# Optimization experiments

Hardware: AMD Instinct MI355X
Metric: run time of the kernel (lower is better)

The kernel has to match this reference:

```python
import jax, jax.numpy as jnp
import numpy as np

N, E = 50000, 1600000
IN_DIM, EMBED, OUT = 512, 128, 64


def setup_inputs() -> dict:
    key = jax.random.key(0)
    k = jax.random.split(key, 8)
    x = jax.random.normal(k[0], (N, IN_DIM), dtype=jnp.float32)
    edge_index = jax.random.randint(k[1], (2, E), 0, N, dtype=jnp.int32)
    W_dense = jax.random.normal(k[2], (EMBED, IN_DIM), dtype=jnp.float32) * 0.02
    b_dense = jnp.zeros((EMBED,), dtype=jnp.float32)
    W_gat = jax.random.normal(k[3], (OUT, EMBED), dtype=jnp.float32) * 0.05
    att_src = jax.random.normal(k[4], (OUT,), dtype=jnp.float32) * 0.1
    att_dst = jax.random.normal(k[5], (OUT,), dtype=jnp.float32) * 0.1
    b_gat = jnp.zeros((OUT,), dtype=jnp.float32)
    return {"x": x, "edge_index": edge_index, "W_dense": W_dense, "b_dense": b_dense,
            "W_gat": W_gat, "att_src": att_src, "att_dst": att_dst, "b_gat": b_gat}


def reference(x, edge_index, W_dense, b_dense, W_gat, att_src, att_dst, b_gat):
    # dense -> LeakyReLU(0.01) (nn.LeakyReLU default)
    h = jax.nn.leaky_relu(x @ W_dense.T + b_dense, negative_slope=0.01)  # [N, EMBED]
    n = h.shape[0]
    # GATConv (PyG, heads=1, add_self_loops=True, negative_slope=0.2)
    loops = jnp.arange(n, dtype=edge_index.dtype)
    src = jnp.concatenate([edge_index[0], loops])
    dst = jnp.concatenate([edge_index[1], loops])
    g = h @ W_gat.T  # [N, OUT]
    a_src = g @ att_src  # [N]
    a_dst = g @ att_dst  # [N]
    e = jax.nn.leaky_relu(a_src[src] + a_dst[dst], negative_slope=0.2)  # [E+N]
    # segment softmax over destination neighborhoods (self loops guarantee non-empty)
    m = jax.ops.segment_max(e, dst, num_segments=n)
    e = jnp.exp(e - m[dst])
    denom = jax.ops.segment_sum(e, dst, num_segments=n)
    alpha = e / denom[dst]
    out = jax.ops.segment_sum(g[src] * alpha[:, None], dst, num_segments=n) + b_gat
    # original returns ([embed_x], [embed_x]); we return the single embedding tensor
    return out
```

## Files before the change

### kernel.cpp

```cpp
#include <hip/hip_runtime.h>
#include <math.h>

#define IN_DIM 512
#define EMBED 128
#define OUT_DIM 64
#define NBPAD 256
#define SEGSH 12
#define CAP_LDS 10240

typedef __attribute__((ext_vector_type(8))) short bf16x8;
typedef __attribute__((ext_vector_type(4))) float f32x4;

__device__ __forceinline__ float lrelu(float v, float s) { return v > 0.f ? v : v * s; }

__device__ __forceinline__ float readlane_f(float v, int l) {
  return __int_as_float(__builtin_amdgcn_readlane(__float_as_int(v), l));
}

__device__ __forceinline__ unsigned short f2bf(float f) {
  unsigned int u = __float_as_uint(f);
  u += 0x7fff + ((u >> 16) & 1);
  return (unsigned short)(u >> 16);
}
__device__ __forceinline__ float bf2f(unsigned short h) {
  return __uint_as_float(((unsigned int)h) << 16);
}

#define LDA 40

__global__ __launch_bounds__(256) void gemm1_mfma_kernel(
    const float* __restrict__ x, const float* __restrict__ Wd,
    const float* __restrict__ bd, float* __restrict__ h, int N) {
  __shared__ __align__(16) unsigned short Ah[128][LDA];
  __shared__ __align__(16) unsigned short Al[128][LDA];
  __shared__ __align__(16) unsigned short Bh[64][LDA];
  __shared__ __align__(16) unsigned short Bl[64][LDA];

  const int tid = threadIdx.x;
  const int lane = tid & 63;
  const int wid = tid >> 6;
  const int wr = wid >> 1, wc = wid & 1;
  const int mblk = blockIdx.x * 128;
  const int nblk = blockIdx.y * 64;
  const int quad = lane >> 4;
  const int l15 = lane & 15;

  const int arow = tid >> 1, acb = (tid & 1) * 16;
  const int brow = tid >> 2, bcb = (tid & 3) * 8;
  const bool avalid = (mblk + arow) < N;
  const float* aptr = x + (size_t)(mblk + arow) * IN_DIM + acb;
  const float* bptr = Wd + (size_t)(nblk + brow) * IN_DIM + bcb;

  f32x4 acc[4][2];
#pragma unroll
  for (int i = 0; i < 4; ++i)
#pragma unroll
    for (int j = 0; j < 2; ++j) acc[i][j] = (f32x4){0.f, 0.f, 0.f, 0.f};

  float4 t0, t1, t2, t3, u0, u1;
  auto do_load = [&](int k0) {
    if (avalid) {
      t0 = *(const float4*)(aptr + k0);
      t1 = *(const float4*)(aptr + k0 + 4);
      t2 = *(const float4*)(aptr + k0 + 8);
      t3 = *(const float4*)(aptr + k0 + 12);
    } else {
      t0 = t1 = t2 = t3 = make_float4(0.f, 0.f, 0.f, 0.f);
    }
    u0 = *(const float4*)(bptr + k0);
    u1 = *(const float4*)(bptr + k0 + 4);
  };
  do_load(0);

  for (int k0 = 0; k0 < IN_DIM; k0 += 32) {
    float av[16] = {t0.x, t0.y, t0.z, t0.w, t1.x, t1.y, t1.z, t1.w,
                    t2.x, t2.y, t2.z, t2.w, t3.x, t3.y, t3.z, t3.w};
    union { unsigned short us[16]; uint4 v[2]; } AH, AL;
#pragma unroll
    for (int i = 0; i < 16; ++i) {
      unsigned short hi = f2bf(av[i]);
      AH.us[i] = hi;
      AL.us[i] = f2bf(av[i] - bf2f(hi));
    }
    float bv[8] = {u0.x, u0.y, u0.z, u0.w, u1.x, u1.y, u1.z, u1.w};
    union { unsigned short us[8]; uint4 v; } BH, BL;
#pragma unroll
    for (int i = 0; i < 8; ++i) {
      unsigned short hi = f2bf(bv[i]);
      BH.us[i] = hi;
      BL.us[i] = f2bf(bv[i] - bf2f(hi));
    }

    __syncthreads();
    *(uint4*)&Ah[arow][acb] = AH.v[0];
    *(uint4*)&Ah[arow][acb + 8] = AH.v[1];
    *(uint4*)&Al[arow][acb] = AL.v[0];
    *(uint4*)&Al[arow][acb + 8] = AL.v[1];
    *(uint4*)&Bh[brow][bcb] = BH.v;
    *(uint4*)&Bl[brow][bcb] = BL.v;
    __syncthreads();

    if (k0 + 32 < IN_DIM) do_load(k0 + 32);

    bf16x8 ah[4], al[4], bh[2], bl[2];
#pragma unroll
    for (int mi = 0; mi < 4; ++mi) {
      int r = wr * 64 + mi * 16 + l15;
      ah[mi] = *(const bf16x8*)&Ah[r][quad * 8];
      al[mi] = *(const bf16x8*)&Al[r][quad * 8];
    }
#pragma unroll
    for (int ni = 0; ni < 2; ++ni) {
      int r = wc * 32 + ni * 16 + l15;
      bh[ni] = *(const bf16x8*)&Bh[r][quad * 8];
      bl[ni] = *(const bf16x8*)&Bl[r][quad * 8];
    }
#pragma unroll
    for (int mi = 0; mi < 4; ++mi)
#pragma unroll
      for (int ni = 0; ni < 2; ++ni) {
        acc[mi][ni] = __builtin_amdgcn_mfma_f32_16x16x32_bf16(ah[mi], bh[ni], acc[mi][ni], 0, 0, 0);
        acc[mi][ni] = __builtin_amdgcn_mfma_f32_16x16x32_bf16(al[mi], bh[ni], acc[mi][ni], 0, 0, 0);
        acc[mi][ni] = __builtin_amdgcn_mfma_f32_16x16x32_bf16(ah[mi], bl[ni], acc[mi][ni], 0, 0, 0);
      }
  }

#pragma unroll
  for (int mi = 0; mi < 4; ++mi)
#pragma unroll
    for (int ni = 0; ni < 2; ++ni) {
      int n = nblk + wc * 32 + ni * 16 + l15;
      float b = bd[n];
#pragma unroll
      for (int r = 0; r < 4; ++r) {
        int m = mblk + wr * 64 + mi * 16 + quad * 4 + r;
        if (m < N) h[(size_t)m * EMBED + n] = lrelu(acc[mi][ni][r] + b, 0.01f);
      }
    }
}

__global__ __launch_bounds__(256) void gemm2_mfma_kernel(
    const float* __restrict__ h, const float* __restrict__ Wg,
    const float* __restrict__ att_src, const float* __restrict__ att_dst,
    float* __restrict__ g, float* __restrict__ a_src, float* __restrict__ a_dst,
    int N) {
  __shared__ __align__(16) unsigned short Ah[128][LDA];
  __shared__ __align__(16) unsigned short Al[128][LDA];
  __shared__ __align__(16) unsigned short Bh[64][LDA];
  __shared__ __align__(16) unsigned short Bl[64][LDA];

  const int tid = threadIdx.x;
  const int lane = tid & 63;
  const int wid = tid >> 6;
  const int wr = wid >> 1, wc = wid & 1;
  const int mblk = blockIdx.x * 128;
  const int quad = lane >> 4;
  const int l15 = lane & 15;

  const int arow = tid >> 1, acb = (tid & 1) * 16;
  const int brow = tid >> 2, bcb = (tid & 3) * 8;
  const bool avalid = (mblk + arow) < N;
  const float* aptr = h + (size_t)(mblk + arow) * EMBED + acb;
  const float* bptr = Wg + (size_t)brow * EMBED + bcb;

  f32x4 acc[4][2];
#pragma unroll
  for (int i = 0; i < 4; ++i)
#pragma unroll
    for (int j = 0; j < 2; ++j) acc[i][j] = (f32x4){0.f, 0.f, 0.f, 0.f};

  float4 t0, t1, t2, t3, u0, u1;
  auto do_load = [&](int k0) {
    if (avalid) {
      t0 = *(const float4*)(aptr + k0);
      t1 = *(const float4*)(aptr + k0 + 4);
      t2 = *(const float4*)(aptr + k0 + 8);
      t3 = *(const float4*)(aptr + k0 + 12);
    } else {
      t0 = t1 = t2 = t3 = make_float4(0.f, 0.f, 0.f, 0.f);
    }
    u0 = *(const float4*)(bptr + k0);
    u1 = *(const float4*)(bptr + k0 + 4);
  };
  do_load(0);

  for (int k0 = 0; k0 < EMBED; k0 += 32) {
    float av[16] = {t0.x, t0.y, t0.z, t0.w, t1.x, t1.y, t1.z, t1.w,
                    t2.x, t2.y, t2.z, t2.w, t3.x, t3.y, t3.z, t3.w};
    union { unsigned short us[16]; uint4 v[2]; } AH, AL;
#pragma unroll
    for (int i = 0; i < 16; ++i) {
      unsigned short hi = f2bf(av[i]);
      AH.us[i] = hi;
      AL.us[i] = f2bf(av[i] - bf2f(hi));
    }
    float bv[8] = {u0.x, u0.y, u0.z, u0.w, u1.x, u1.y, u1.z, u1.w};
    union { unsigned short us[8]; uint4 v; } BH, BL;
#pragma unroll
    for (int i = 0; i < 8; ++i) {
      unsigned short hi = f2bf(bv[i]);
      BH.us[i] = hi;
      BL.us[i] = f2bf(bv[i] - bf2f(hi));
    }

    __syncthreads();
    *(uint4*)&Ah[arow][acb] = AH.v[0];
    *(uint4*)&Ah[arow][acb + 8] = AH.v[1];
    *(uint4*)&Al[arow][acb] = AL.v[0];
    *(uint4*)&Al[arow][acb + 8] = AL.v[1];
    *(uint4*)&Bh[brow][bcb] = BH.v;
    *(uint4*)&Bl[brow][bcb] = BL.v;
    __syncthreads();

    if (k0 + 32 < EMBED) do_load(k0 + 32);

    bf16x8 ah[4], al[4], bh[2], bl[2];
#pragma unroll
    for (int mi = 0; mi < 4; ++mi) {
      int r = wr * 64 + mi * 16 + l15;
      ah[mi] = *(const bf16x8*)&Ah[r][quad * 8];
      al[mi] = *(const bf16x8*)&Al[r][quad * 8];
    }
#pragma unroll
    for (int ni = 0; ni < 2; ++ni) {
      int r = wc * 32 + ni * 16 + l15;
      bh[ni] = *(const bf16x8*)&Bh[r][quad * 8];
      bl[ni] = *(const bf16x8*)&Bl[r][quad * 8];
    }
#pragma unroll
    for (int mi = 0; mi < 4; ++mi)
#pragma unroll
      for (int ni = 0; ni < 2; ++ni) {
        acc[mi][ni] = __builtin_amdgcn_mfma_f32_16x16x32_bf16(ah[mi], bh[ni], acc[mi][ni], 0, 0, 0);
        acc[mi][ni] = __builtin_amdgcn_mfma_f32_16x16x32_bf16(al[mi], bh[ni], acc[mi][ni], 0, 0, 0);
        acc[mi][ni] = __builtin_amdgcn_mfma_f32_16x16x32_bf16(ah[mi], bl[ni], acc[mi][ni], 0, 0, 0);
      }
  }

  float as_[2], ad_[2];
#pragma unroll
  for (int ni = 0; ni < 2; ++ni) {
    int n = wc * 32 + ni * 16 + l15;
    as_[ni] = att_src[n];
    ad_[ni] = att_dst[n];
  }
#pragma unroll
  for (int mi = 0; mi < 4; ++mi) {
#pragma unroll
    for (int r = 0; r < 4; ++r) {
      int m = mblk + wr * 64 + mi * 16 + quad * 4 + r;
      float ps = acc[mi][0][r] * as_[0] + acc[mi][1][r] * as_[1];
      float pd = acc[mi][0][r] * ad_[0] + acc[mi][1][r] * ad_[1];
#pragma unroll
      for (int d = 1; d < 16; d <<= 1) {
        ps += __shfl_xor(ps, d, 64);
        pd += __shfl_xor(pd, d, 64);
      }
      if (m < N) {
#pragma unroll
        for (int ni = 0; ni < 2; ++ni) {
          int n = wc * 32 + ni * 16 + l15;
          g[(size_t)m * OUT_DIM + n] = acc[mi][ni][r];
        }
        if (l15 == 0 && wc == 0) {
          a_src[m] = ps;
          a_dst[m] = pd;
        }
      }
    }
  }
  __syncthreads();
#pragma unroll
  for (int mi = 0; mi < 4; ++mi) {
#pragma unroll
    for (int r = 0; r < 4; ++r) {
      int m = mblk + wr * 64 + mi * 16 + quad * 4 + r;
      float ps = acc[mi][0][r] * as_[0] + acc[mi][1][r] * as_[1];
      float pd = acc[mi][0][r] * ad_[0] + acc[mi][1][r] * ad_[1];
#pragma unroll
      for (int d = 1; d < 16; d <<= 1) {
        ps += __shfl_xor(ps, d, 64);
        pd += __shfl_xor(pd, d, 64);
      }
      if (m < N && l15 == 0 && wc == 1) {
        atomicAdd(&a_src[m], ps);
        atomicAdd(&a_dst[m], pd);
      }
    }
  }
}

__global__ __launch_bounds__(256) void hist_count_kernel(
    const int* __restrict__ ei, int* __restrict__ histT, int nblkP, int E,
    int N) {
  __shared__ int cnt[NBPAD];
  const int t = threadIdx.x;
  cnt[t] = 0;
  __syncthreads();
  const int T = E + N;
  const int base = blockIdx.x << SEGSH;
#pragma unroll
  for (int q = 0; q < (1 << SEGSH) / 256; ++q) {
    int i = base + q * 256 + t;
    if (i < T) {
      int d = (i < E) ? ei[E + i] : (i - E);
      atomicAdd(&cnt[d >> 8], 1);
    }
  }
  __syncthreads();
  histT[(size_t)t * nblkP + blockIdx.x] = cnt[t];
}

__global__ __launch_bounds__(256) void row_scan_kernel(
    int* __restrict__ histT, int* __restrict__ bucket_tot, int nblkP) {
  __shared__ int sc[256];
  const int t = threadIdx.x;
  int* row = histT + (size_t)blockIdx.x * nblkP;
  const int per = (nblkP + 255) / 256;
  int loc[8];
  int sum = 0;
#pragma unroll 4
  for (int j = 0; j < per; ++j) {
    int idx = t * per + j;
    int v = (idx < nblkP) ? row[idx] : 0;
    loc[j] = sum;
    sum += v;
  }
  sc[t] = sum;
  __syncthreads();
  for (int dlt = 1; dlt < 256; dlt <<= 1) {
    int add = (t >= dlt) ? sc[t - dlt] : 0;
    __syncthreads();
    sc[t] += add;
    __syncthreads();
  }
  const int off = sc[t] - sum;
#pragma unroll 4
  for (int j = 0; j < per; ++j) {
    int idx = t * per + j;
    if (idx < nblkP) row[idx] = off + loc[j];
  }
  if (t == 255) bucket_tot[blockIdx.x] = sc[255];
}

__global__ __launch_bounds__(256) void base_scan_kernel(
    const int* __restrict__ bucket_tot, int* __restrict__ bucket_base,
    int* __restrict__ offsets, int N, int T) {
  __shared__ int sc[256];
  const int t = threadIdx.x;
  int v = bucket_tot[t];
  sc[t] = v;
  __syncthreads();
  for (int dlt = 1; dlt < 256; dlt <<= 1) {
    int add = (t >= dlt) ? sc[t - dlt] : 0;
    __syncthreads();
    sc[t] += add;
    __syncthreads();
  }
  bucket_base[t] = sc[t] - v;
  if (t == 0) offsets[N] = T;
}

__global__ __launch_bounds__(256) void bin_kernel(
    const int* __restrict__ ei, const int* __restrict__ histT,
    const int* __restrict__ bucket_base, int* __restrict__ stageB, int nblkP,
    int E, int N) {
  __shared__ int cnt[NBPAD];
  __shared__ int basev[NBPAD];
  const int t = threadIdx.x;
  cnt[t] = 0;
  basev[t] = bucket_base[t] + histT[(size_t)t * nblkP + blockIdx.x];
  __syncthreads();
  const int T = E + N;
  const int base = blockIdx.x << SEGSH;
#pragma unroll
  for (int q = 0; q < (1 << SEGSH) / 256; ++q) {
    int i = base + q * 256 + t;
    if (i < T) {
      int s, d;
      if (i < E) {
        s = ei[i];
        d = ei[E + i];
      } else {
        s = d = i - E;
      }
      int b = d >> 8;
      int r = atomicAdd(&cnt[b], 1);
      stageB[basev[b] + r] = (s << 8) | (d & 255);
    }
  }
}

__global__ __launch_bounds__(256) void build_kernel(
    const int* __restrict__ stageB, const int* __restrict__ bucket_base,
    const int* __restrict__ bucket_tot, const float* __restrict__ a_src,
    const float* __restrict__ a_dst, int* __restrict__ offsets,
    int2* __restrict__ csr_pack, int N) {
  __shared__ int cnt[256];
  __shared__ int pre[256];
  __shared__ int cur[256];
  __shared__ int2 buf[CAP_LDS];
  const int b = blockIdx.x;
  const int t = threadIdx.x;
  const int base = bucket_base[b];
  const int tot = bucket_tot[b];
  cnt[t] = 0;
  __syncthreads();
  const int* sp = stageB + base;
  for (int i = t; i < tot; i += 256) atomicAdd(&cnt[sp[i] & 255], 1);
  __syncthreads();
  int v = cnt[t];
  pre[t] = v;
  __syncthreads();
  for (int dlt = 1; dlt < 256; dlt <<= 1) {
    int add = (t >= dlt) ? pre[t - dlt] : 0;
    __syncthreads();
    pre[t] += add;
    __syncthreads();
  }
  const int excl = pre[t] - v;
  cur[t] = excl;
  const int d_self = (b << 8) | t;
  if (d_self < N) offsets[d_self] = base + excl;
  __syncthreads();
  for (int i = t; i < tot; i += 256) {
    int rec = sp[i];
    int dl = rec & 255;
    int s = rec >> 8;
    float e = a_src[s] + a_dst[(b << 8) | dl];
    e = e > 0.f ? e : 0.2f * e;
    int pos = atomicAdd(&cur[dl], 1);
    int2 r2 = make_int2(s, __float_as_int(e));
    if (pos < CAP_LDS)
      buf[pos] = r2;
    else
      csr_pack[base + pos] = r2;
  }
  __syncthreads();
  const int lim = min(tot, CAP_LDS);
  for (int i = t; i < lim; i += 256) csr_pack[base + i] = buf[i];
}

__global__ __launch_bounds__(256) void aggregate_kernel(
    const int* __restrict__ offsets, const int2* __restrict__ csr_pack,
    const float* __restrict__ g, const float* __restrict__ b_gat,
    float* __restrict__ out, int N) {
  const int lane = threadIdx.x & 63;
  const int node = blockIdx.x * 4 + (threadIdx.x >> 6);
  if (node >= N) return;
  const int beg = offsets[node], end = offsets[node + 1];

  float m = -1e30f;
  for (int j = beg + lane; j < end; j += 64)
    m = fmaxf(m, __int_as_float(csr_pack[j].y));
#pragma unroll
  for (int d = 1; d < 64; d <<= 1) m = fmaxf(m, __shfl_xor(m, d, 64));

  float l = 0.f;
  for (int j = beg + lane; j < end; j += 64)
    l += __expf(__int_as_float(csr_pack[j].y) - m);
#pragma unroll
  for (int d = 1; d < 64; d <<= 1) l += __shfl_xor(l, d, 64);
  const float inv_l = 1.f / l;

  float acc0 = 0.f, acc1 = 0.f, acc2 = 0.f, acc3 = 0.f;
  for (int jb = beg; jb < end; jb += 64) {
    int j = jb + lane;
    float p = 0.f;
    int s = 0;
    if (j < end) {
      int2 rec = csr_pack[j];
      p = __expf(__int_as_float(rec.y) - m) * inv_l;
      s = rec.x;
    }
    const int cnt = min(64, end - jb);
    int jj = 0;
    for (; jj + 4 <= cnt; jj += 4) {
      int s0 = __builtin_amdgcn_readlane(s, jj);
      int s1 = __builtin_amdgcn_readlane(s, jj + 1);
      int s2 = __builtin_amdgcn_readlane(s, jj + 2);
      int s3 = __builtin_amdgcn_readlane(s, jj + 3);
      float p0 = readlane_f(p, jj);
      float p1 = readlane_f(p, jj + 1);
      float p2 = readlane_f(p, jj + 2);
      float p3 = readlane_f(p, jj + 3);
      acc0 += p0 * g[((size_t)s0 << 6) + lane];
      acc1 += p1 * g[((size_t)s1 << 6) + lane];
      acc2 += p2 * g[((size_t)s2 << 6) + lane];
      acc3 += p3 * g[((size_t)s3 << 6) + lane];
    }
    for (; jj < cnt; ++jj) {
      int s0 = __builtin_amdgcn_readlane(s, jj);
      float p0 = readlane_f(p, jj);
      acc0 += p0 * g[((size_t)s0 << 6) + lane];
    }
  }
  out[(size_t)node * OUT_DIM + lane] = (acc0 + acc1) + (acc2 + acc3) + b_gat[lane];
}

extern "C" void kernel_launch(void* const* d_in, const int* in_sizes, int n_in,
                              void* d_out, int out_size, void* d_ws, size_t ws_size,
                              hipStream_t stream) {
  const float* x = (const float*)d_in[0];
  const int* ei = (const int*)d_in[1];
  const float* Wd = (const float*)d_in[2];
  const float* bd = (const float*)d_in[3];
  const float* Wg = (const float*)d_in[4];
  const float* att_src = (const float*)d_in[5];
  const float* att_dst = (const float*)d_in[6];
  const float* bg = (const float*)d_in[7];
  float* out = (float*)d_out;

  const int N = in_sizes[0] / IN_DIM;
  const int E = in_sizes[1] / 2;
  const int T = E + N;
  const int NB = (N + 255) >> 8;
  const int nblkP = (T + (1 << SEGSH) - 1) >> SEGSH;

  char* ws = (char*)d_ws;
  size_t off = 0;
  auto alloc = [&](size_t bytes) -> void* {
    void* p = ws + off;
    off += (bytes + 15) & ~(size_t)15;
    return p;
  };
  float* h = (float*)alloc((size_t)N * EMBED * 4);
  float* g = (float*)alloc((size_t)N * OUT_DIM * 4);
  float* a_src = (float*)alloc((size_t)N * 4);
  float* a_dst = (float*)alloc((size_t)N * 4);
  int* offsets = (int*)alloc((size_t)(N + 1) * 4);
  int* histT = (int*)alloc((size_t)NBPAD * nblkP * 4);
  int* bucket_base = (int*)alloc((size_t)NBPAD * 4);
  int* bucket_tot = (int*)alloc((size_t)NBPAD * 4);
  int* stageB = (int*)alloc((size_t)T * 4);
  int2* csr_pack = (int2*)alloc((size_t)T * 8);

  hipLaunchKernelGGL(gemm1_mfma_kernel, dim3((N + 127) / 128, 2), dim3(256), 0,
                     stream, x, Wd, bd, h, N);
  hipLaunchKernelGGL(gemm2_mfma_kernel, dim3((N + 127) / 128), dim3(256), 0,
                     stream, h, Wg, att_src, att_dst, g, a_src, a_dst, N);
  hipLaunchKernelGGL(hist_count_kernel, dim3(nblkP), dim3(256), 0, stream,
                     ei, histT, nblkP, E, N);
  hipLaunchKernelGGL(row_scan_kernel, dim3(NBPAD), dim3(256), 0, stream,
                     histT, bucket_tot, nblkP);
  hipLaunchKernelGGL(base_scan_kernel, dim3(1), dim3(256), 0, stream,
                     bucket_tot, bucket_base, offsets, N, T);
  hipLaunchKernelGGL(bin_kernel, dim3(nblkP), dim3(256), 0, stream,
                     ei, histT, bucket_base, stageB, nblkP, E, N);
  hipLaunchKernelGGL(build_kernel, dim3(NB), dim3(256), 0, stream,
                     stageB, bucket_base, bucket_tot, a_src, a_dst, offsets,
                     csr_pack, N);
  hipLaunchKernelGGL(aggregate_kernel, dim3((N + 3) / 4), dim3(256), 0, stream,
                     offsets, csr_pack, g, bg, out, N);
}
```

Measured before the change: 320.0 us.

## Pre-split dense weights to bf16 hi/lo and shrink gemm1 M-tile

Adds a small kernel that splits W_dense once per call into bf16 high and low parts, so gemm1 loads ready bf16 weights instead of converting fp32 weights in every block. The fp32-to-bf16 split of x now uses the packed v_cvt_pk_bf16_f32 instruction rather than manual rounding arithmetic. The gemm1 M-tile shrinks from 128 to 64 rows, which doubles the grid and lowers per-thread conversion work and register use. In exchange it adds an extra kernel launch and re-reads the weights from more blocks. The packed conversion's rounding may also differ slightly from the manual round-to-nearest-even.

New measurement: 329.9 us. 1.03x slower.

```diff
diff --git a/kernel.cpp b/kernel.cpp
--- a/kernel.cpp
+++ b/kernel.cpp
@@ -26,13 +26,40 @@
   return __uint_as_float(((unsigned int)h) << 16);
 }
 
+__device__ __forceinline__ unsigned int cvt_pk_bf16(float a, float b) {
+  unsigned int r;
+  asm("v_cvt_pk_bf16_f32 %0, %1, %2" : "=v"(r) : "v"(a), "v"(b));
+  return r;
+}
+
 #define LDA 40
 
+__global__ __launch_bounds__(256) void split_w_kernel(
+    const float* __restrict__ W, unsigned short* __restrict__ Wh,
+    unsigned short* __restrict__ Wl, int total) {
+  int i = (blockIdx.x * 256 + threadIdx.x) * 4;
+  if (i >= total) return;
+  float4 v = *(const float4*)(W + i);
+  unsigned int h0 = cvt_pk_bf16(v.x, v.y);
+  unsigned int h1 = cvt_pk_bf16(v.z, v.w);
+  float r0 = v.x - __uint_as_float(h0 << 16);
+  float r1 = v.y - __uint_as_float(h0 & 0xffff0000u);
+  float r2 = v.z - __uint_as_float(h1 << 16);
+  float r3 = v.w - __uint_as_float(h1 & 0xffff0000u);
+  unsigned int l0 = cvt_pk_bf16(r0, r1);
+  unsigned int l1 = cvt_pk_bf16(r2, r3);
+  uint2 hh = make_uint2(h0, h1);
+  uint2 ll = make_uint2(l0, l1);
+  *(uint2*)(Wh + i) = hh;
+  *(uint2*)(Wl + i) = ll;
+}
+
 __global__ __launch_bounds__(256) void gemm1_mfma_kernel(
-    const float* __restrict__ x, const float* __restrict__ Wd,
-    const float* __restrict__ bd, float* __restrict__ h, int N) {
-  __shared__ __align__(16) unsigned short Ah[128][LDA];
-  __shared__ __align__(16) unsigned short Al[128][LDA];
+    const float* __restrict__ x, const unsigned short* __restrict__ Wdh,
+    const unsigned short* __restrict__ Wdl, const float* __restrict__ bd,
+    float* __restrict__ h, int N) {
+  __shared__ __align__(16) unsigned short Ah[64][LDA];
+  __shared__ __align__(16) unsigned short Al[64][LDA];
   __shared__ __align__(16) unsigned short Bh[64][LDA];
   __shared__ __align__(16) unsigned short Bl[64][LDA];
 
@@ -40,72 +67,62 @@
   const int lane = tid & 63;
   const int wid = tid >> 6;
   const int wr = wid >> 1, wc = wid & 1;
-  const int mblk = blockIdx.x * 128;
+  const int mblk = blockIdx.x * 64;
   const int nblk = blockIdx.y * 64;
   const int quad = lane >> 4;
   const int l15 = lane & 15;
 
-  const int arow = tid >> 1, acb = (tid & 1) * 16;
-  const int brow = tid >> 2, bcb = (tid & 3) * 8;
+  const int arow = tid >> 2, acb = (tid & 3) * 8;
   const bool avalid = (mblk + arow) < N;
   const float* aptr = x + (size_t)(mblk + arow) * IN_DIM + acb;
-  const float* bptr = Wd + (size_t)(nblk + brow) * IN_DIM + bcb;
-
-  f32x4 acc[4][2];
-#pragma unroll
-  for (int i = 0; i < 4; ++i)
+  const unsigned short* bhp = Wdh + (size_t)(nblk + arow) * IN_DIM + acb;
+  const unsigned short* blp = Wdl + (size_t)(nblk + arow) * IN_DIM + acb;
+
+  f32x4 acc[2][2];
+#pragma unroll
+  for (int i = 0; i < 2; ++i)
 #pragma unroll
     for (int j = 0; j < 2; ++j) acc[i][j] = (f32x4){0.f, 0.f, 0.f, 0.f};
 
-  float4 t0, t1, t2, t3, u0, u1;
+  float4 t0, t1;
+  uint4 bhv, blv;
   auto do_load = [&](int k0) {
     if (avalid) {
       t0 = *(const float4*)(aptr + k0);
       t1 = *(const float4*)(aptr + k0 + 4);
-      t2 = *(const float4*)(aptr + k0 + 8);
-      t3 = *(const float4*)(aptr + k0 + 12);
     } else {
-      t0 = t1 = t2 = t3 = make_float4(0.f, 0.f, 0.f, 0.f);
-    }
-    u0 = *(const float4*)(bptr + k0);
-    u1 = *(const float4*)(bptr + k0 + 4);
+      t0 = t1 = make_float4(0.f, 0.f, 0.f, 0.f);
+    }
+    bhv = *(const uint4*)(bhp + k0);
+    blv = *(const uint4*)(blp + k0);
   };
   do_load(0);
 
   for (int k0 = 0; k0 < IN_DIM; k0 += 32) {
-    float av[16] = {t0.x, t0.y, t0.z, t0.w, t1.x, t1.y, t1.z, t1.w,
-                    t2.x, t2.y, t2.z, t2.w, t3.x, t3.y, t3.z, t3.w};
-    union { unsigned short us[16]; uint4 v[2]; } AH, AL;
-#pragma unroll
-    for (int i = 0; i < 16; ++i) {
-      unsigned short hi = f2bf(av[i]);
-      AH.us[i] = hi;
-      AL.us[i] = f2bf(av[i] - bf2f(hi));
-    }
-    float bv[8] = {u0.x, u0.y, u0.z, u0.w, u1.x, u1.y, u1.z, u1.w};
-    union { unsigned short us[8]; uint4 v; } BH, BL;
-#pragma unroll
-    for (int i = 0; i < 8; ++i) {
-      unsigned short hi = f2bf(bv[i]);
-      BH.us[i] = hi;
-      BL.us[i] = f2bf(bv[i] - bf2f(hi));
-    }
-
-    __syncthreads();
-    *(uint4*)&Ah[arow][acb] = AH.v[0];
-    *(uint4*)&Ah[arow][acb + 8] = AH.v[1];
-    *(uint4*)&Al[arow][acb] = AL.v[0];
-    *(uint4*)&Al[arow][acb + 8] = AL.v[1];
-    *(uint4*)&Bh[brow][bcb] = BH.v;
-    *(uint4*)&Bl[brow][bcb] = BL.v;
+    float av[8] = {t0.x, t0.y, t0.z, t0.w, t1.x, t1.y, t1.z, t1.w};
+    union { unsigned int u[4]; uint4 v; } AHI, ALO;
+#pragma unroll
+    for (int i = 0; i < 4; ++i) {
+      unsigned int hp = cvt_pk_bf16(av[2 * i], av[2 * i + 1]);
+      float r0 = av[2 * i] - __uint_as_float(hp << 16);
+      float r1 = av[2 * i + 1] - __uint_as_float(hp & 0xffff0000u);
+      AHI.u[i] = hp;
+      ALO.u[i] = cvt_pk_bf16(r0, r1);
+    }
+
+    __syncthreads();
+    *(uint4*)&Ah[arow][acb] = AHI.v;
+    *(uint4*)&Al[arow][acb] = ALO.v;
+    *(uint4*)&Bh[arow][acb] = bhv;
+    *(uint4*)&Bl[arow][acb] = blv;
     __syncthreads();
 
     if (k0 + 32 < IN_DIM) do_load(k0 + 32);
 
-    bf16x8 ah[4], al[4], bh[2], bl[2];
-#pragma unroll
-    for (int mi = 0; mi < 4; ++mi) {
-      int r = wr * 64 + mi * 16 + l15;
+    bf16x8 ah[2], al[2], bh[2], bl[2];
+#pragma unroll
+    for (int mi = 0; mi < 2; ++mi) {
+      int r = wr * 32 + mi * 16 + l15;
       ah[mi] = *(const bf16x8*)&Ah[r][quad * 8];
       al[mi] = *(const bf16x8*)&Al[r][quad * 8];
     }
@@ -116,7 +133,7 @@
       bl[ni] = *(const bf16x8*)&Bl[r][quad * 8];
     }
 #pragma unroll
-    for (int mi = 0; mi < 4; ++mi)
+    for (int mi = 0; mi < 2; ++mi)
 #pragma unroll
       for (int ni = 0; ni < 2; ++ni) {
         acc[mi][ni] = __builtin_amdgcn_mfma_f32_16x16x32_bf16(ah[mi], bh[ni], acc[mi][ni], 0, 0, 0);
@@ -126,14 +143,14 @@
   }
 
 #pragma unroll
-  for (int mi = 0; mi < 4; ++mi)
+  for (int mi = 0; mi < 2; ++mi)
 #pragma unroll
     for (int ni = 0; ni < 2; ++ni) {
       int n = nblk + wc * 32 + ni * 16 + l15;
       float b = bd[n];
 #pragma unroll
       for (int r = 0; r < 4; ++r) {
-        int m = mblk + wr * 64 + mi * 16 + quad * 4 + r;
+        int m = mblk + wr * 32 + mi * 16 + quad * 4 + r;
         if (m < N) h[(size_t)m * EMBED + n] = lrelu(acc[mi][ni][r] + b, 0.01f);
       }
     }
@@ -534,9 +551,14 @@
   int* bucket_tot = (int*)alloc((size_t)NBPAD * 4);
   int* stageB = (int*)alloc((size_t)T * 4);
   int2* csr_pack = (int2*)alloc((size_t)T * 8);
-
-  hipLaunchKernelGGL(gemm1_mfma_kernel, dim3((N + 127) / 128, 2), dim3(256), 0,
-                     stream, x, Wd, bd, h, N);
+  unsigned short* Wdh = (unsigned short*)alloc((size_t)EMBED * IN_DIM * 2);
+  unsigned short* Wdl = (unsigned short*)alloc((size_t)EMBED * IN_DIM * 2);
+
+  const int WTOT = EMBED * IN_DIM;
+  hipLaunchKernelGGL(split_w_kernel, dim3(WTOT / 1024), dim3(256), 0, stream,
+                     Wd, Wdh, Wdl, WTOT);
+  hipLaunchKernelGGL(gemm1_mfma_kernel, dim3((N + 63) / 64, 2), dim3(256), 0,
+                     stream, x, Wdh, Wdl, bd, h, N);
   hipLaunchKernelGGL(gemm2_mfma_kernel, dim3((N + 127) / 128), dim3(256), 0,
                      stream, h, Wg, att_src, att_dst, g, a_src, a_dst, N);
   hipLaunchKernelGGL(hist_count_kernel, dim3(nblkP), dim3(256), 0, stream,
```
